# Optimization experiments

Measured on AMD Instinct MI355X. Metric: run time of the kernel, lower is better.

## Reference

```python
import jax, jax.numpy as jnp
import numpy as np

C = 512
B, H, W = 8, 64, 64
GROUPS = 32
EPS = 1e-6


def setup_inputs() -> dict:
    key = jax.random.key(0)
    ks = jax.random.split(key, 6)
    s = 1.0 / np.sqrt(C)
    return {
        "x": jax.random.normal(ks[0], (B, C, H, W), dtype=jnp.float32),
        "gn_scale": jnp.ones((C,), jnp.float32),
        "gn_bias": jnp.zeros((C,), jnp.float32),
        "wq": jax.random.normal(ks[1], (C, C), jnp.float32) * s,
        "bq": jnp.zeros((C,), jnp.float32),
        "wk": jax.random.normal(ks[2], (C, C), jnp.float32) * s,
        "bk": jnp.zeros((C,), jnp.float32),
        "wv": jax.random.normal(ks[3], (C, C), jnp.float32) * s,
        "bv": jnp.zeros((C,), jnp.float32),
        "wo": jax.random.normal(ks[4], (C, C), jnp.float32) * s,
        "bo": jnp.zeros((C,), jnp.float32),
    }


def group_norm(x, scale, bias):
    # x: [b, c, h, w]; GroupNorm(32 groups, eps=1e-6, affine)
    b, c, h, w = x.shape
    xg = x.reshape(b, GROUPS, c // GROUPS, h, w)
    mean = xg.mean(axis=(2, 3, 4), keepdims=True)
    var = xg.var(axis=(2, 3, 4), keepdims=True)
    xg = (xg - mean) * jax.lax.rsqrt(var + EPS)
    return xg.reshape(b, c, h, w) * scale[None, :, None, None] + bias[None, :, None, None]


def reference(x, gn_scale, gn_bias, wq, bq, wk, bk, wv, bv, wo, bo):
    b, c, h, w = x.shape
    n = h * w
    hn = group_norm(x, gn_scale, gn_bias).reshape(b, c, n)  # [b,c,n]
    # 1x1 convs == channel matmuls
    q = jnp.einsum('oc,bcn->bon', wq, hn) + bq[None, :, None]
    k = jnp.einsum('oc,bcn->bon', wk, hn) + bk[None, :, None]
    v = jnp.einsum('oc,bcn->bon', wv, hn) + bv[None, :, None]
    # scores: [b, n_query, n_key], softmax over keys
    scores = jnp.einsum('bcn,bcm->bnm', q, k) * (float(c) ** -0.5)
    attn = jax.nn.softmax(scores, axis=2)
    # out[b,c,i] = sum_j v[b,c,j] * attn[b,i,j]
    out = jnp.einsum('bcm,bnm->bcn', v, attn)
    out = jnp.einsum('oc,bcn->bon', wo, out) + bo[None, :, None]
    return x + out.reshape(b, c, h, w)
```

## Files before the change

kernel.cpp:

```cpp
#include <hip/hip_runtime.h>
#include <hip/hip_bf16.h>


typedef __bf16 bf16_t;
typedef __bf16 bf16x8 __attribute__((ext_vector_type(8)));
typedef __bf16 bf16x4 __attribute__((ext_vector_type(4)));
typedef float  f32x4  __attribute__((ext_vector_type(4)));

#define CDIM 512
#define NSP  4096
#define L2E  1.4426950408889634f

typedef __attribute__((address_space(1))) const void* as1_cvp;
typedef __attribute__((address_space(3))) void*       as3_vp;

__device__ __forceinline__ void gload_lds16(const void* g, void* l) {
  __builtin_amdgcn_global_load_lds((as1_cvp)g, (as3_vp)l, 16, 0, 0);
}

__global__ __launch_bounds__(256) void f32_to_bf16_k(const float* __restrict__ in,
                                                     bf16_t* __restrict__ out, int n) {
  int i = (blockIdx.x * 256 + threadIdx.x) * 4;
  if (i < n) {
    float4 v = *(const float4*)(in + i);
    bf16x4 o;
    o[0] = (bf16_t)v.x; o[1] = (bf16_t)v.y; o[2] = (bf16_t)v.z; o[3] = (bf16_t)v.w;
    *(bf16x4*)(out + i) = o;
  }
}

__global__ __launch_bounds__(256) void gn_stats_k(const float* __restrict__ x,
                                                  float* __restrict__ stats) {
  const int gid = blockIdx.x;
  const float4* base = (const float4*)(x + (long)gid * 65536);
  float s = 0.f, ss = 0.f;
  for (int i = threadIdx.x; i < 16384; i += 256) {
    float4 t = base[i];
    s  += t.x + t.y + t.z + t.w;
    ss += t.x*t.x + t.y*t.y + t.z*t.z + t.w*t.w;
  }
#pragma unroll
  for (int o = 32; o; o >>= 1) { s += __shfl_xor(s, o); ss += __shfl_xor(ss, o); }
  __shared__ float rs[4], rss[4];
  const int lane = threadIdx.x & 63, wid = threadIdx.x >> 6;
  if (lane == 0) { rs[wid] = s; rss[wid] = ss; }
  __syncthreads();
  if (threadIdx.x == 0) {
    s  = rs[0] + rs[1] + rs[2] + rs[3];
    ss = rss[0] + rss[1] + rss[2] + rss[3];
    float mean = s * (1.f / 65536.f);
    float var  = ss * (1.f / 65536.f) - mean * mean;
    stats[gid]       = mean;
    stats[256 + gid] = rsqrtf(var + 1e-6f);
  }
}

__global__ __launch_bounds__(256) void gn_apply_k(const float* __restrict__ x,
                                                  const float* __restrict__ stats,
                                                  const float* __restrict__ gw,
                                                  const float* __restrict__ gb,
                                                  bf16_t* __restrict__ hnT) {
  __shared__ float tile[64 * 65];
  const int n0 = blockIdx.x * 64;
  const int c0 = blockIdx.y * 64;
  const int b  = blockIdx.z;
  const int tid = threadIdx.x;
  {
    const int cl = tid >> 2, nq = tid & 3;
    const int c = c0 + cl;
    const int g = c >> 4;
    const float mean = stats[b * 32 + g];
    const float rstd = stats[256 + b * 32 + g];
    const float a  = rstd * gw[c];
    const float bb = gb[c] - mean * a;
    const float4* xr = (const float4*)(x + ((long)b * CDIM + c) * NSP + n0 + nq * 16);
#pragma unroll
    for (int i = 0; i < 4; i++) {
      float4 t = xr[i];
      float* d = &tile[cl * 65 + nq * 16 + i * 4];
      d[0] = t.x * a + bb; d[1] = t.y * a + bb; d[2] = t.z * a + bb; d[3] = t.w * a + bb;
    }
  }
  __syncthreads();
  {
    const int nl = tid >> 2, cq = tid & 3;
    union { bf16_t h[16]; uint4 v[2]; } o;
#pragma unroll
    for (int j = 0; j < 16; j++) o.h[j] = (bf16_t)tile[(cq * 16 + j) * 65 + nl];
    bf16_t* dst = hnT + ((long)b * NSP + n0 + nl) * CDIM + c0 + cq * 16;
    ((uint4*)dst)[0] = o.v[0];
    ((uint4*)dst)[1] = o.v[1];
  }
}

template <int MODE>
__global__ __launch_bounds__(256) void gemm_bt_k(
    const bf16_t* __restrict__ A, long sAb, long ldA,
    const bf16_t* __restrict__ B, long sBb, long ldB,
    void* __restrict__ Cout, long sCb, long ldC, void* __restrict__ Cout2,
    int M, int N, int K,
    const float* __restrict__ bias_row,
    const float* __restrict__ bias_col,
    float scale,
    const float* __restrict__ residual, long sRb) {
  __shared__ __align__(16) bf16_t sA[128 * 32];
  __shared__ __align__(16) bf16_t sB[128 * 32];

  const int tid  = threadIdx.x;
  const int lane = tid & 63;
  const int wid  = tid >> 6;
  const int wm = wid >> 1, wn = wid & 1;
  const int b = blockIdx.z;
  const int rowBase = blockIdx.y * 128;
  const int colBase = blockIdx.x * 128;

  const bf16_t* Ab = A + (long)b * sAb + (long)rowBase * ldA;
  const bf16_t* Bb = B + (long)b * sBb + (long)colBase * ldB;

  f32x4 acc[4][4];
#pragma unroll
  for (int i = 0; i < 4; i++)
#pragma unroll
    for (int j = 0; j < 4; j++) acc[i][j] = (f32x4){0.f, 0.f, 0.f, 0.f};

  const int q0 = tid, q1 = tid + 256;
  const int r0 = q0 >> 2, k0c = (q0 & 3) * 8;
  const int r1 = q1 >> 2, k1c = (q1 & 3) * 8;
  const int mrow  = lane & 15;
  const int kfrag = (lane >> 4) * 8;

  for (int kt = 0; kt < K; kt += 32) {
    gload_lds16(Ab + (long)r0 * ldA + kt + k0c, sA + q0 * 8);
    gload_lds16(Ab + (long)r1 * ldA + kt + k1c, sA + q1 * 8);
    gload_lds16(Bb + (long)r0 * ldB + kt + k0c, sB + q0 * 8);
    gload_lds16(Bb + (long)r1 * ldB + kt + k1c, sB + q1 * 8);
    __syncthreads();
    bf16x8 af[4], bfr[4];
#pragma unroll
    for (int t = 0; t < 4; t++) {
      af[t]  = *(const bf16x8*)&sA[(wm * 64 + t * 16 + mrow) * 32 + kfrag];
      bfr[t] = *(const bf16x8*)&sB[(wn * 64 + t * 16 + mrow) * 32 + kfrag];
    }
#pragma unroll
    for (int i = 0; i < 4; i++)
#pragma unroll
      for (int j = 0; j < 4; j++)
        acc[i][j] = __builtin_amdgcn_mfma_f32_16x16x32_bf16(af[i], bfr[j], acc[i][j], 0, 0, 0);
    __syncthreads();
  }

  const int quad = lane >> 4;
  const int colf = lane & 15;
#pragma unroll
  for (int i = 0; i < 4; i++) {
#pragma unroll
    for (int j = 0; j < 4; j++) {
#pragma unroll
      for (int r = 0; r < 4; r++) {
        const int row = rowBase + wm * 64 + i * 16 + quad * 4 + r;
        const int col = colBase + wn * 64 + j * 16 + colf;
        float v = acc[i][j][r];
        if (MODE == 2) {
          if (col < 512)
            ((bf16_t*)Cout)[(long)b * sCb + (long)row * ldC + col] =
                (bf16_t)((v + bias_col[col]) * scale);
          else
            ((bf16_t*)Cout2)[(long)b * sCb + (long)row * ldC + (col - 512)] =
                (bf16_t)(v + bias_row[col - 512]);
        } else {
          if (bias_row) v += bias_row[row];
          if (bias_col) v += bias_col[col];
          v *= scale;
          if (residual) v += residual[(long)b * sRb + (long)row * ldC + col];
          if (MODE == 1)
            ((bf16_t*)Cout)[(long)b * sCb + (long)row * ldC + col] = (bf16_t)v;
          else
            ((float*)Cout)[(long)b * sCb + (long)row * ldC + col] = v;
        }
      }
    }
  }
}

__device__ __forceinline__ void stage_k(const bf16_t* __restrict__ Kb, int j0, int h,
                                        bf16_t* dst, int tid) {
#pragma unroll
  for (int i = 0; i < 8; ++i) {
    const int e = i * 2048 + tid * 8;
    const int row = e >> 8;
    const int slot = (e >> 3) & 31;
    gload_lds16(Kb + (long)(j0 + row) * CDIM + h * 256 + ((slot ^ (row & 7)) << 3),
                dst + e);
  }
}

__device__ __forceinline__ void stage_v(const bf16_t* __restrict__ Vb, int j0, int h,
                                        bf16_t* dst, int tid) {
#pragma unroll
  for (int i = 0; i < 8; ++i) {
    const int e = i * 2048 + tid * 8;
    const int row = e >> 6;
    const int slot = (e >> 3) & 7;
    gload_lds16(Vb + (long)(h * 256 + row) * NSP + j0 + ((slot ^ (row & 7)) << 3),
                dst + e);
  }
}

#define PH_WAIT8() do { asm volatile("s_waitcnt vmcnt(8)\n\ts_barrier" ::: "memory"); \
                        __builtin_amdgcn_sched_barrier(0); } while (0)
#define PH_WAIT0() do { asm volatile("s_waitcnt vmcnt(0)\n\ts_barrier" ::: "memory"); \
                        __builtin_amdgcn_sched_barrier(0); } while (0)
#define PH_END()   do { asm volatile("s_barrier" ::: "memory"); \
                        __builtin_amdgcn_sched_barrier(0); } while (0)

__global__ __launch_bounds__(256, 2) void flash_attn_k(
    const bf16_t* __restrict__ QT, const bf16_t* __restrict__ KT,
    const bf16_t* __restrict__ V, bf16_t* __restrict__ O1T) {
  __shared__ __align__(16) bf16_t sBuf[2][16384];
  __shared__ __align__(16) bf16_t sP[4][16 * 72];

  const int tid = threadIdx.x, lane = tid & 63, w = tid >> 6;
  const int quad = lane >> 4, l15 = lane & 15;
  const int sw = l15 & 7;
  const int bid = blockIdx.x;
  const int b = bid & 7;
  const int q0 = (bid >> 3) * 64;

  const bf16_t* Qw = QT + ((long)b * NSP + q0 + w * 16) * CDIM;
  const bf16_t* Kb = KT + (long)b * NSP * CDIM;
  const bf16_t* Vb = V  + (long)b * NSP * CDIM;

  stage_k(Kb, 0, 0, &sBuf[0][0], tid);

  bf16x8 qf[16];
#pragma unroll
  for (int kc = 0; kc < 16; kc++)
    qf[kc] = *(const bf16x8*)(Qw + (long)l15 * CDIM + kc * 32 + quad * 8);

  bf16x8 vone;
#pragma unroll
  for (int j = 0; j < 8; j++) vone[j] = (bf16_t)1.0f;

  f32x4 oacc[32];
#pragma unroll
  for (int i = 0; i < 32; i++) oacc[i] = (f32x4){0.f, 0.f, 0.f, 0.f};
  float m_r[4] = {-3e38f, -3e38f, -3e38f, -3e38f};
  f32x4 lacc = (f32x4){0.f, 0.f, 0.f, 0.f};

#pragma unroll 1
  for (int it = 0; it < 64; ++it) {
    const int j0 = it * 64;
    f32x4 sacc[4];
#pragma unroll
    for (int t = 0; t < 4; t++) sacc[t] = (f32x4){0.f, 0.f, 0.f, 0.f};
    bf16x8 pf0, pf1;

    stage_k(Kb, j0, 1, &sBuf[1][0], tid);
    PH_WAIT8();
    __builtin_amdgcn_s_setprio(1);
#pragma unroll
    for (int kc = 0; kc < 8; kc++) {
#pragma unroll
      for (int t = 0; t < 4; t++) {
        const bf16x8 kf = *(const bf16x8*)(
            &sBuf[0][(t * 16 + l15) * 256 + (((kc * 4 + quad) ^ sw) << 3)]);
        sacc[t] = __builtin_amdgcn_mfma_f32_16x16x32_bf16(qf[kc], kf, sacc[t], 0, 0, 0);
      }
    }
    __builtin_amdgcn_s_setprio(0);
    PH_END();

    stage_v(Vb, j0, 0, &sBuf[0][0], tid);
    PH_WAIT8();
    __builtin_amdgcn_s_setprio(1);
#pragma unroll
    for (int kc = 8; kc < 16; kc++) {
#pragma unroll
      for (int t = 0; t < 4; t++) {
        const bf16x8 kf = *(const bf16x8*)(
            &sBuf[1][(t * 16 + l15) * 256 + ((((kc - 8) * 4 + quad) ^ sw) << 3)]);
        sacc[t] = __builtin_amdgcn_mfma_f32_16x16x32_bf16(qf[kc], kf, sacc[t], 0, 0, 0);
      }
    }
    __builtin_amdgcn_s_setprio(0);

    {
      f32x4 av;
#pragma unroll
      for (int r = 0; r < 4; r++) {
        float mx = fmaxf(fmaxf(sacc[0][r], sacc[1][r]), fmaxf(sacc[2][r], sacc[3][r]));
        mx = fmaxf(mx, __shfl_xor(mx, 1));
        mx = fmaxf(mx, __shfl_xor(mx, 2));
        mx = fmaxf(mx, __shfl_xor(mx, 4));
        mx = fmaxf(mx, __shfl_xor(mx, 8));
        const float mn = fmaxf(m_r[r], mx);
        av[r] = exp2f((m_r[r] - mn) * L2E);
        m_r[r] = mn;
#pragma unroll
        for (int t = 0; t < 4; t++)
          sacc[t][r] = exp2f((sacc[t][r] - mn) * L2E);
      }
#pragma unroll
      for (int i = 0; i < 32; i++) oacc[i] *= av;
      lacc *= av;
#pragma unroll
      for (int t = 0; t < 4; t++)
#pragma unroll
        for (int r = 0; r < 4; r++)
          sP[w][(quad * 4 + r) * 72 + t * 16 + l15] = (bf16_t)sacc[t][r];
    }
    pf0 = *(const bf16x8*)(&sP[w][l15 * 72 + quad * 8]);
    pf1 = *(const bf16x8*)(&sP[w][l15 * 72 + 32 + quad * 8]);
    lacc = __builtin_amdgcn_mfma_f32_16x16x32_bf16(pf0, vone, lacc, 0, 0, 0);
    lacc = __builtin_amdgcn_mfma_f32_16x16x32_bf16(pf1, vone, lacc, 0, 0, 0);
    PH_END();

    stage_v(Vb, j0, 1, &sBuf[1][0], tid);
    PH_WAIT8();
    __builtin_amdgcn_s_setprio(1);
#pragma unroll
    for (int ct = 0; ct < 16; ct++) {
      const int row = ct * 16 + l15;
      const bf16x8 vf0 = *(const bf16x8*)(&sBuf[0][row * 64 + ((quad ^ sw) << 3)]);
      const bf16x8 vf1 = *(const bf16x8*)(&sBuf[0][row * 64 + (((4 + quad) ^ sw) << 3)]);
      oacc[ct] = __builtin_amdgcn_mfma_f32_16x16x32_bf16(pf0, vf0, oacc[ct], 0, 0, 0);
      oacc[ct] = __builtin_amdgcn_mfma_f32_16x16x32_bf16(pf1, vf1, oacc[ct], 0, 0, 0);
    }
    __builtin_amdgcn_s_setprio(0);
    PH_END();

    if (it < 63) {
      stage_k(Kb, j0 + 64, 0, &sBuf[0][0], tid);
      PH_WAIT8();
    } else {
      PH_WAIT0();
    }
    __builtin_amdgcn_s_setprio(1);
#pragma unroll
    for (int ct = 0; ct < 16; ct++) {
      const int row = ct * 16 + l15;
      const bf16x8 vf0 = *(const bf16x8*)(&sBuf[1][row * 64 + ((quad ^ sw) << 3)]);
      const bf16x8 vf1 = *(const bf16x8*)(&sBuf[1][row * 64 + (((4 + quad) ^ sw) << 3)]);
      oacc[16 + ct] = __builtin_amdgcn_mfma_f32_16x16x32_bf16(pf0, vf0, oacc[16 + ct], 0, 0, 0);
      oacc[16 + ct] = __builtin_amdgcn_mfma_f32_16x16x32_bf16(pf1, vf1, oacc[16 + ct], 0, 0, 0);
    }
    __builtin_amdgcn_s_setprio(0);
    PH_END();
  }

  const f32x4 linv = {1.f / lacc[0], 1.f / lacc[1], 1.f / lacc[2], 1.f / lacc[3]};
  bf16_t* sO = &sBuf[0][0];
#pragma unroll
  for (int ct = 0; ct < 32; ct++) {
    const f32x4 o = oacc[ct] * linv;
#pragma unroll
    for (int r = 0; r < 4; r++)
      sO[(w * 16 + quad * 4 + r) * 512 + ct * 16 + l15] = (bf16_t)o[r];
  }
  __syncthreads();
  bf16_t* Ob = O1T + ((long)b * NSP + q0) * CDIM;
#pragma unroll
  for (int i = 0; i < 16; i++) {
    const int g = i * 256 + tid, row = g >> 6, off = g & 63;
    *(uint4*)(Ob + (long)row * CDIM + off * 8) = *(const uint4*)(sO + row * 512 + off * 8);
  }
}

extern "C" void kernel_launch(void* const* d_in, const int* in_sizes, int n_in,
                              void* d_out, int out_size, void* d_ws, size_t ws_size,
                              hipStream_t stream) {
  const float* x        = (const float*)d_in[0];
  const float* gn_scale = (const float*)d_in[1];
  const float* gn_bias  = (const float*)d_in[2];
  const float* wq = (const float*)d_in[3];
  const float* bq = (const float*)d_in[4];
  const float* wk = (const float*)d_in[5];
  const float* bk = (const float*)d_in[6];
  const float* wv = (const float*)d_in[7];
  const float* bv = (const float*)d_in[8];
  const float* wo = (const float*)d_in[9];
  const float* bo = (const float*)d_in[10];
  float* out = (float*)d_out;

  const long PB = 2097152;
  const long MB = 1048576L;
  char* w = (char*)d_ws;
  bf16_t* hnT  = (bf16_t*)(w);
  bf16_t* O1T  = hnT;
  bf16_t* QT   = (bf16_t*)(w + 32 * MB);
  bf16_t* KT   = (bf16_t*)(w + 64 * MB);
  bf16_t* V    = (bf16_t*)(w + 96 * MB);
  bf16_t* wqkb = (bf16_t*)(w + 128 * MB);
  bf16_t* wvb  = (bf16_t*)(w + 129 * MB);
  bf16_t* wob  = (bf16_t*)(w + 129 * MB + 524288L);
  float*  stats = (float*)(w + 130 * MB);

  const float qscale = 0.044194173824159216f;

  f32_to_bf16_k<<<256, 256, 0, stream>>>(wq, wqkb, 262144);
  f32_to_bf16_k<<<256, 256, 0, stream>>>(wk, wqkb + 262144, 262144);
  f32_to_bf16_k<<<256, 256, 0, stream>>>(wv, wvb, 262144);
  f32_to_bf16_k<<<256, 256, 0, stream>>>(wo, wob, 262144);

  gn_stats_k<<<256, 256, 0, stream>>>(x, stats);
  gn_apply_k<<<dim3(64, 8, 8), 256, 0, stream>>>(x, stats, gn_scale, gn_bias, hnT);

  gemm_bt_k<2><<<dim3(8, 32, 8), 256, 0, stream>>>(
      hnT, PB, 512, wqkb, 0, 512, QT, PB, 512, KT, 4096, 1024, 512,
      bk, bq, qscale, nullptr, 0);
  gemm_bt_k<1><<<dim3(32, 4, 8), 256, 0, stream>>>(
      wvb, 0, 512, hnT, PB, 512, V, PB, 4096, nullptr, 512, 4096, 512,
      bv, nullptr, 1.f, nullptr, 0);

  flash_attn_k<<<dim3(512), 256, 0, stream>>>(QT, KT, V, O1T);

  gemm_bt_k<0><<<dim3(32, 4, 8), 256, 0, stream>>>(
      wob, 0, 512, O1T, PB, 512, (void*)out, PB, 4096, nullptr, 512, 4096, 512,
      bo, nullptr, 1.f, x, PB);
}
```

Baseline: 1.079 ms.

## Repartition PV matmul across waves by channel using 32x32 MFMA tiles

The P·V product is restructured so each wave owns a 64-channel slice for all 64 queries, using 32x32x16 MFMA instead of 16x16x32 with per-wave query rows. The softmax P tile is shared through one block-wide LDS buffer, and per-row rescale factors and final normalizers pass through a new sAlpha LDS array. This is meant to cut redundant V fragment reads from LDS, since each wave now reads only its channel slice, and to use larger MFMA tiles. In exchange it adds cross-wave LDS traffic for P and alpha, a __syncthreads at the end, and a scattered output layout.

```diff
diff --git a/kernel.cpp b/kernel.cpp
--- a/kernel.cpp
+++ b/kernel.cpp
@@ -6,6 +6,7 @@
 typedef __bf16 bf16x8 __attribute__((ext_vector_type(8)));
 typedef __bf16 bf16x4 __attribute__((ext_vector_type(4)));
 typedef float  f32x4  __attribute__((ext_vector_type(4)));
+typedef float  f32x16 __attribute__((ext_vector_type(16)));
 
 #define CDIM 512
 #define NSP  4096
@@ -217,10 +218,12 @@
     const bf16_t* __restrict__ QT, const bf16_t* __restrict__ KT,
     const bf16_t* __restrict__ V, bf16_t* __restrict__ O1T) {
   __shared__ __align__(16) bf16_t sBuf[2][16384];
-  __shared__ __align__(16) bf16_t sP[4][16 * 72];
+  __shared__ __align__(16) bf16_t sP[64 * 72];
+  __shared__ __align__(16) float  sAlpha[64];
 
   const int tid = threadIdx.x, lane = tid & 63, w = tid >> 6;
   const int quad = lane >> 4, l15 = lane & 15;
+  const int l31 = lane & 31, ls = lane >> 5;
   const int sw = l15 & 7;
   const int bid = blockIdx.x;
   const int b = bid & 7;
@@ -241,9 +244,16 @@
 #pragma unroll
   for (int j = 0; j < 8; j++) vone[j] = (bf16_t)1.0f;
 
-  f32x4 oacc[32];
-#pragma unroll
-  for (int i = 0; i < 32; i++) oacc[i] = (f32x4){0.f, 0.f, 0.f, 0.f};
+  f32x16 oacc16[2][2][2];
+#pragma unroll
+  for (int mt = 0; mt < 2; mt++)
+#pragma unroll
+    for (int h = 0; h < 2; h++)
+#pragma unroll
+      for (int nt = 0; nt < 2; nt++)
+#pragma unroll
+        for (int e = 0; e < 16; e++) oacc16[mt][h][nt][e] = 0.f;
+
   float m_r[4] = {-3e38f, -3e38f, -3e38f, -3e38f};
   f32x4 lacc = (f32x4){0.f, 0.f, 0.f, 0.f};
 
@@ -253,7 +263,6 @@
     f32x4 sacc[4];
 #pragma unroll
     for (int t = 0; t < 4; t++) sacc[t] = (f32x4){0.f, 0.f, 0.f, 0.f};
-    bf16x8 pf0, pf1;
 
     stage_k(Kb, j0, 1, &sBuf[1][0], tid);
     PH_WAIT8();
@@ -300,31 +309,59 @@
         for (int t = 0; t < 4; t++)
           sacc[t][r] = exp2f((sacc[t][r] - mn) * L2E);
       }
-#pragma unroll
-      for (int i = 0; i < 32; i++) oacc[i] *= av;
+      if (l15 == 0) {
+#pragma unroll
+        for (int r = 0; r < 4; r++) sAlpha[w * 16 + quad * 4 + r] = av[r];
+      }
       lacc *= av;
 #pragma unroll
       for (int t = 0; t < 4; t++)
 #pragma unroll
         for (int r = 0; r < 4; r++)
-          sP[w][(quad * 4 + r) * 72 + t * 16 + l15] = (bf16_t)sacc[t][r];
-    }
-    pf0 = *(const bf16x8*)(&sP[w][l15 * 72 + quad * 8]);
-    pf1 = *(const bf16x8*)(&sP[w][l15 * 72 + 32 + quad * 8]);
-    lacc = __builtin_amdgcn_mfma_f32_16x16x32_bf16(pf0, vone, lacc, 0, 0, 0);
-    lacc = __builtin_amdgcn_mfma_f32_16x16x32_bf16(pf1, vone, lacc, 0, 0, 0);
+          sP[(w * 16 + quad * 4 + r) * 72 + t * 16 + l15] = (bf16_t)sacc[t][r];
+    }
+    {
+      const bf16x8 pf0 = *(const bf16x8*)(&sP[(w * 16 + l15) * 72 + quad * 8]);
+      const bf16x8 pf1 = *(const bf16x8*)(&sP[(w * 16 + l15) * 72 + 32 + quad * 8]);
+      lacc = __builtin_amdgcn_mfma_f32_16x16x32_bf16(pf0, vone, lacc, 0, 0, 0);
+      lacc = __builtin_amdgcn_mfma_f32_16x16x32_bf16(pf1, vone, lacc, 0, 0, 0);
+    }
     PH_END();
 
     stage_v(Vb, j0, 1, &sBuf[1][0], tid);
     PH_WAIT8();
+#pragma unroll
+    for (int mt = 0; mt < 2; mt++) {
+      f32x16 av;
+#pragma unroll
+      for (int rq = 0; rq < 4; rq++) {
+        const f32x4 a4 = *(const f32x4*)&sAlpha[mt * 32 + rq * 8 + ls * 4];
+        av[rq * 4 + 0] = a4[0];
+        av[rq * 4 + 1] = a4[1];
+        av[rq * 4 + 2] = a4[2];
+        av[rq * 4 + 3] = a4[3];
+      }
+#pragma unroll
+      for (int h = 0; h < 2; h++)
+#pragma unroll
+        for (int nt = 0; nt < 2; nt++)
+          oacc16[mt][h][nt] *= av;
+    }
     __builtin_amdgcn_s_setprio(1);
 #pragma unroll
-    for (int ct = 0; ct < 16; ct++) {
-      const int row = ct * 16 + l15;
-      const bf16x8 vf0 = *(const bf16x8*)(&sBuf[0][row * 64 + ((quad ^ sw) << 3)]);
-      const bf16x8 vf1 = *(const bf16x8*)(&sBuf[0][row * 64 + (((4 + quad) ^ sw) << 3)]);
-      oacc[ct] = __builtin_amdgcn_mfma_f32_16x16x32_bf16(pf0, vf0, oacc[ct], 0, 0, 0);
-      oacc[ct] = __builtin_amdgcn_mfma_f32_16x16x32_bf16(pf1, vf1, oacc[ct], 0, 0, 0);
+    for (int s = 0; s < 4; s++) {
+      const bf16x8 pA0 = *(const bf16x8*)&sP[l31 * 72 + s * 16 + ls * 8];
+      const bf16x8 pA1 = *(const bf16x8*)&sP[(32 + l31) * 72 + s * 16 + ls * 8];
+#pragma unroll
+      for (int nt = 0; nt < 2; nt++) {
+        const int cl = w * 64 + nt * 32 + l31;
+        const bf16x8 vB = *(const bf16x8*)
+            &sBuf[0][cl * 64 + (((s * 2 + ls) ^ (cl & 7)) << 3)];
+        oacc16[0][0][nt] =
+            __builtin_amdgcn_mfma_f32_32x32x16_bf16(pA0, vB, oacc16[0][0][nt], 0, 0, 0);
+        oacc16[1][0][nt] =
+            __builtin_amdgcn_mfma_f32_32x32x16_bf16(pA1, vB, oacc16[1][0][nt], 0, 0, 0);
+      }
     }
     __builtin_amdgcn_s_setprio(0);
     PH_END();
@@ -337,25 +374,53 @@
     }
     __builtin_amdgcn_s_setprio(1);
 #pragma unroll
-    for (int ct = 0; ct < 16; ct++) {
-      const int row = ct * 16 + l15;
-      const bf16x8 vf0 = *(const bf16x8*)(&sBuf[1][row * 64 + ((quad ^ sw) << 3)]);
-      const bf16x8 vf1 = *(const bf16x8*)(&sBuf[1][row * 64 + (((4 + quad) ^ sw) << 3)]);
-      oacc[16 + ct] = __builtin_amdgcn_mfma_f32_16x16x32_bf16(pf0, vf0, oacc[16 + ct], 0, 0, 0);
-      oacc[16 + ct] = __builtin_amdgcn_mfma_f32_16x16x32_bf16(pf1, vf1, oacc[16 + ct], 0, 0, 0);
+    for (int s = 0; s < 4; s++) {
+      const bf16x8 pA0 = *(const bf16x8*)&sP[l31 * 72 + s * 16 + ls * 8];
+      const bf16x8 pA1 = *(const bf16x8*)&sP[(32 + l31) * 72 + s * 16 + ls * 8];
+#pragma unroll
+      for (int nt = 0; nt < 2; nt++) {
+        const int cl = w * 64 + nt * 32 + l31;
+        const bf16x8 vB = *(const bf16x8*)
+            &sBuf[1][cl * 64 + (((s * 2 + ls) ^ (cl & 7)) << 3)];
+        oacc16[0][1][nt] =
+            __builtin_amdgcn_mfma_f32_32x32x16_bf16(pA0, vB, oacc16[0][1][nt], 0, 0, 0);
+        oacc16[1][1][nt] =
+            __builtin_amdgcn_mfma_f32_32x32x16_bf16(pA1, vB, oacc16[1][1][nt], 0, 0, 0);
+      }
     }
     __builtin_amdgcn_s_setprio(0);
     PH_END();
   }
 
-  const f32x4 linv = {1.f / lacc[0], 1.f / lacc[1], 1.f / lacc[2], 1.f / lacc[3]};
+  if (l15 == 0) {
+#pragma unroll
+    for (int r = 0; r < 4; r++) sAlpha[w * 16 + quad * 4 + r] = lacc[r];
+  }
+  __syncthreads();
   bf16_t* sO = &sBuf[0][0];
 #pragma unroll
-  for (int ct = 0; ct < 32; ct++) {
-    const f32x4 o = oacc[ct] * linv;
-#pragma unroll
-    for (int r = 0; r < 4; r++)
-      sO[(w * 16 + quad * 4 + r) * 512 + ct * 16 + l15] = (bf16_t)o[r];
+  for (int mt = 0; mt < 2; mt++) {
+    f32x16 linv;
+#pragma unroll
+    for (int rq = 0; rq < 4; rq++) {
+      const f32x4 l4 = *(const f32x4*)&sAlpha[mt * 32 + rq * 8 + ls * 4];
+      linv[rq * 4 + 0] = 1.f / l4[0];
+      linv[rq * 4 + 1] = 1.f / l4[1];
+      linv[rq * 4 + 2] = 1.f / l4[2];
+      linv[rq * 4 + 3] = 1.f / l4[3];
+    }
+#pragma unroll
+    for (int h = 0; h < 2; h++)
+#pragma unroll
+      for (int nt = 0; nt < 2; nt++) {
+        const f32x16 o = oacc16[mt][h][nt] * linv;
+        const int c = h * 256 + w * 64 + nt * 32 + l31;
+#pragma unroll
+        for (int reg = 0; reg < 16; reg++) {
+          const int row = mt * 32 + (reg & 3) + 8 * (reg >> 2) + 4 * ls;
+          sO[row * 512 + c] = (bf16_t)o[reg];
+        }
+      }
   }
   __syncthreads();
   bf16_t* Ob = O1T + ((long)b * NSP + q0) * CDIM;
```

After: 1.489 ms. 1.38x slower.
